# Optimization experiments

Measured on AMD Instinct MI355X. Metric: run time of the kernel, lower is better.

Reference implementation:

```python
import jax, jax.numpy as jnp
import numpy as np

P = 7            # cfg.PATCH_SIZE_PHOTOMETRIC
BRIGHT = 0.02    # bright_threshold
BIG = 1e9        # masks invalid points out of kNN
K = 5            # neighbors for smoothness/slope


def _smooth_l1(x, y, beta):
    d = jnp.abs(x - y)
    return jnp.where(d < beta, 0.5 * d * d / beta, d - 0.5 * beta)


def _sample_patches(img, kp):
    # img: [B,1,H,W], kp: [B,N,2] (x,y) in pixel coords -> [B,1,N,P,P]
    # matches F.grid_sample(align_corners=True, bilinear, border): with the
    # module's normalization, sampling positions are exactly pixel coords.
    B, _, H, W = img.shape
    N = kp.shape[1]
    half = P // 2
    lin = jnp.linspace(-half, half, P)
    oy, ox = jnp.meshgrid(lin, lin, indexing='ij')  # patch index (i,j): +x=lin[j], +y=lin[i]
    px = jnp.clip(kp[..., 0:1] + ox.ravel(), 0.0, W - 1)  # [B,N,P*P]
    py = jnp.clip(kp[..., 1:2] + oy.ravel(), 0.0, H - 1)
    x0 = jnp.floor(px); y0 = jnp.floor(py)
    fx = px - x0; fy = py - y0
    x0i = jnp.clip(x0.astype(jnp.int32), 0, W - 1)
    x1i = jnp.clip(x0i + 1, 0, W - 1)
    y0i = jnp.clip(y0.astype(jnp.int32), 0, H - 1)
    y1i = jnp.clip(y0i + 1, 0, H - 1)
    im = img[:, 0]  # [B,H,W]
    b = jnp.arange(B)[:, None, None]
    v00 = im[b, y0i, x0i]; v01 = im[b, y0i, x1i]
    v10 = im[b, y1i, x0i]; v11 = im[b, y1i, x1i]
    val = (v00 * (1 - fx) + v01 * fx) * (1 - fy) + (v10 * (1 - fx) + v11 * fx) * fy
    return val.reshape(B, 1, N, P, P)


def _forward(lg, rg, kpl, kpr, scores, Q):
    B, N, _ = kpl.shape
    # ---- epipolar ----
    y_diff = jnp.abs(kpl[..., 1] - kpr[..., 1])
    ws = scores.sum()
    l_epipolar = jnp.where(ws > 1e-4, (y_diff * scores).sum() / jnp.maximum(ws, 1e-12), y_diff.mean())
    # ---- photometric + intensity ----
    pl = _sample_patches(lg, kpl)
    pr = _sample_patches(rg, kpr)
    c = P // 2
    center_l = pl[:, 0, :, c, c]  # [B,N]
    center_r = pr[:, 0, :, c, c]
    is_bright = (center_l > BRIGHT).astype(pl.dtype)
    diff = jnp.abs(pl - pr).mean(axis=(1, 3, 4))  # [B,N]
    w = scores * is_bright
    wsum = w.sum()
    safe = jnp.maximum(wsum, 1e-12)
    l_masked = jnp.where(wsum > 1e-4, (diff * w).sum() / safe, 0.0)
    l_intensity = jnp.where(wsum > 1e-4, (_smooth_l1(center_l, center_r, 1.0) * w).sum() / safe, 0.0)
    l_photo = l_masked + l_intensity
    # ---- disparity -> 3D ----
    disp = kpl[..., 0] - kpr[..., 0]
    pts4 = jnp.concatenate([kpl, disp[..., None], jnp.ones((B, N, 1), kpl.dtype)], axis=-1)
    proj = jnp.einsum('bni,bji->bnj', pts4, Q)
    Wc = jnp.maximum(proj[..., 3], 1e-6)
    p3d = proj[..., :3] / Wc[..., None]  # [B,N,3]
    Z = p3d[..., 2]
    valid = (Z > 100) & (Z < 30000) & (scores > 0.1)  # [B,N]
    # ---- kNN smoothness / slope / zero-mean (masked, vectorized) ----
    pm = p3d / 1000.0
    xy = pm[..., jnp.array([0, 2])]  # [B,N,2] horizontal plane
    h = pm[..., 1]                   # [B,N] height
    sq = (xy * xy).sum(-1)
    d2 = sq[:, :, None] + sq[:, None, :] - 2.0 * jnp.einsum('bnd,bmd->bnm', xy, xy)
    dist = jnp.sqrt(jnp.maximum(d2, 1e-12))  # [B,N,N]
    vm = valid[:, :, None] & valid[:, None, :]
    dist = jnp.where(vm, dist, BIG)
    negd, idx = jax.lax.top_k(-dist, K + 1)   # ascending distance
    nbr_idx = idx[:, :, 1:]                   # drop self
    nbr_d = jnp.maximum(-negd[:, :, 1:], 1e-3)
    b = jnp.arange(B)[:, None, None]
    nbr_h = h[b, nbr_idx]                     # [B,N,K]
    local_mean = nbr_h.mean(-1)
    n_valid = valid.sum(-1)
    nv = jnp.maximum(n_valid, 1).astype(h.dtype)
    vf = valid.astype(h.dtype)
    ls_b = (_smooth_l1(h, local_mean, 0.01) * vf).sum(-1) / nv
    slopes = jnp.abs(nbr_h - h[..., None]) / nbr_d
    pen = jax.nn.relu(slopes - 0.4)
    lsl_b = (pen * vf[..., None]).sum((-1, -2)) / (nv * K)
    lz_b = jnp.abs((h * vf).sum(-1) / nv)
    ok = (n_valid >= 10).astype(h.dtype)
    nb = jnp.maximum(ok.sum(), 1.0)
    gate = ((scores > 0.1).sum() >= 10) & (ok.sum() > 0)
    l_smooth = jnp.where(gate, (ls_b * ok).sum() / nb, 0.0)
    l_slope = jnp.where(gate, (lsl_b * ok).sum() / nb, 0.0)
    l_zeromean = jnp.where(gate, (lz_b * ok).sum() / nb, 0.0)
    return (l_photo, l_epipolar, l_smooth, l_slope, l_zeromean)


def setup_inputs() -> dict:
    key = jax.random.key(0)
    k = jax.random.split(key, 7)
    B, N, H, W = 16, 2000, 720, 1280
    lg = jax.random.uniform(k[0], (B, 1, H, W), dtype=jnp.float32)
    rg = jax.random.uniform(k[1], (B, 1, H, W), dtype=jnp.float32)
    kx = jax.random.uniform(k[2], (B, N), minval=200.0, maxval=1080.0)
    ky = jax.random.uniform(k[3], (B, N), minval=50.0, maxval=670.0)
    disp = jax.random.uniform(k[4], (B, N), minval=10.0, maxval=200.0)
    kpl = jnp.stack([kx, ky], -1)
    kpr = jnp.stack([kx - disp, ky + 0.5 * jax.random.normal(k[5], (B, N))], -1)
    scores = jax.random.uniform(k[6], (B, N), dtype=jnp.float32)
    f, cx, cy, Tx = 1000.0, 640.0, 360.0, 120.0  # focal px, principal point, baseline mm
    Qm = jnp.array([[1.0, 0.0, 0.0, -cx],
                    [0.0, 1.0, 0.0, -cy],
                    [0.0, 0.0, 0.0, f],
                    [0.0, 0.0, 1.0 / Tx, 0.0]], dtype=jnp.float32)
    Q = jnp.broadcast_to(Qm, (B, 4, 4))
    return {"lg": lg, "rg": rg, "kpl": kpl, "kpr": kpr, "scores": scores, "Q": Q}


def reference(lg, rg, kpl, kpr, scores, Q):
    return _forward(lg, rg, kpl, kpr, scores, Q)
```

## Files before the change

kernel.cpp:

```cpp
#include <hip/hip_runtime.h>

#define BB 16
#define NN 2000
#define HH 720
#define WW 1280
#define NPT (BB*NN)
#define PATCH_BLOCKS (NPT/32)
#define PROJ_BLOCKS (NPT/256)
#define KSTRIDE 2048

static __device__ __forceinline__ unsigned u_min(unsigned a, unsigned b){ return a < b ? a : b; }

static __device__ __forceinline__ unsigned u_med3(unsigned a, unsigned b, unsigned c) {
    unsigned d;
    asm("v_med3_u32 %0, %1, %2, %3" : "=v"(d) : "v"(a), "v"(b), "v"(c));
    return d;
}

__device__ __forceinline__ void ins5(unsigned K[5], unsigned u) {
    K[4] = u_med3(K[3], K[4], u);
    K[3] = u_med3(K[2], K[3], u);
    K[2] = u_med3(K[1], K[2], u);
    K[1] = u_med3(K[0], K[1], u);
    K[0] = u_min(K[0], u);
}

__device__ __forceinline__ float bilin(const float* __restrict__ im, float px, float py) {
    px = fminf(fmaxf(px, 0.f), (float)(WW - 1));
    py = fminf(fmaxf(py, 0.f), (float)(HH - 1));
    float x0f = floorf(px), y0f = floorf(py);
    float fx = px - x0f, fy = py - y0f;
    int x0 = min(max((int)x0f, 0), WW - 1);
    int x1 = min(x0 + 1, WW - 1);
    int y0 = min(max((int)y0f, 0), HH - 1);
    int y1 = min(y0 + 1, HH - 1);
    const float* r0 = im + (size_t)y0 * WW;
    const float* r1 = im + (size_t)y1 * WW;
    float v00 = r0[x0], v01 = r0[x1], v10 = r1[x0], v11 = r1[x1];
    return (v00 * (1.f - fx) + v01 * fx) * (1.f - fy)
         + (v10 * (1.f - fx) + v11 * fx) * fy;
}

__global__ __launch_bounds__(256) void project_kernel(
    const float* __restrict__ kpl, const float* __restrict__ kpr,
    const float* __restrict__ scores, const float* __restrict__ Q,
    float4* __restrict__ pts, float* __restrict__ partialsA,
    float* __restrict__ batch_acc, unsigned* __restrict__ dcnt)
{
    if (blockIdx.x == 0) {
        if (threadIdx.x < BB * 4) batch_acc[threadIdx.x] = 0.f;
        if (threadIdx.x == BB * 4) *dcnt = 0u;
    }
    int pt = blockIdx.x * 256 + threadIdx.x;
    int b  = pt / NN;

    float2 kl = ((const float2* __restrict__)kpl)[pt];
    float2 kr = ((const float2* __restrict__)kpr)[pt];
    float sc  = scores[pt];
    float ydiff = fabsf(kl.y - kr.y);

    const float* q = Q + b * 16;
    float dsp = kl.x - kr.x;
    float p0 = q[0]*kl.x  + q[1]*kl.y  + q[2]*dsp  + q[3];
    float p1 = q[4]*kl.x  + q[5]*kl.y  + q[6]*dsp  + q[7];
    float p2 = q[8]*kl.x  + q[9]*kl.y  + q[10]*dsp + q[11];
    float p3 = q[12]*kl.x + q[13]*kl.y + q[14]*dsp + q[15];
    float Wc = fmaxf(p3, 1e-6f);
    float X = p0 / Wc, Y = p1 / Wc, Z = p2 / Wc;
    bool valid = (Z > 100.f) && (Z < 30000.f) && (sc > 0.1f);
    float x  = X / 1000.f;
    float hh = Y / 1000.f;
    float y  = Z / 1000.f;
    float sq = x * x + y * y;
    if (!valid) { x = 0.f; y = 0.f; sq = 1e18f; }
    pts[pt] = make_float4(x, y, sq, hh);

    float s0 = sc, s1 = ydiff * sc, s2 = ydiff, s3 = (sc > 0.1f) ? 1.f : 0.f;
    #pragma unroll
    for (int off = 32; off > 0; off >>= 1) {
        s0 += __shfl_down(s0, off, 64);
        s1 += __shfl_down(s1, off, 64);
        s2 += __shfl_down(s2, off, 64);
        s3 += __shfl_down(s3, off, 64);
    }
    __shared__ float red[4][4];
    int wave = threadIdx.x >> 6, lane = threadIdx.x & 63;
    if (lane == 0) { red[wave][0]=s0; red[wave][1]=s1; red[wave][2]=s2; red[wave][3]=s3; }
    __syncthreads();
    if (threadIdx.x < 4) {
        int k = threadIdx.x;
        partialsA[blockIdx.x * 4 + k] = red[0][k] + red[1][k] + red[2][k] + red[3][k];
    }
}

__global__ __launch_bounds__(256) void fused_patch_scan(
    const float* __restrict__ lg, const float* __restrict__ rg,
    const float* __restrict__ kpl, const float* __restrict__ kpr,
    const float* __restrict__ scores,
    const float4* __restrict__ pts, unsigned* __restrict__ keybuf,
    float* __restrict__ partialsB, int msegLen, int lns)
{
    if (blockIdx.x < PATCH_BLOCKS) {
        int wave = threadIdx.x >> 6, lane = threadIdx.x & 63;
        int rr = lane / 7, ci = lane - rr * 7;
        int s00 = lane + rr;
        if (s00 > 54) s00 = 54;
        int reg_r = lane >> 3, reg_c = lane & 7;

        float a3 = 0.f, a4 = 0.f, a5 = 0.f;

        for (int it = 0; it < 8; ++it) {
            int pt = blockIdx.x * 32 + wave * 8 + it;
            int b = pt / NN;
            const float* iml = lg + (size_t)b * (HH * WW);
            const float* imr = rg + (size_t)b * (HH * WW);
            float kxl = kpl[2*pt], kyl = kpl[2*pt+1];
            float kxr = kpr[2*pt], kyr = kpr[2*pt+1];
            float sc  = scores[pt];

            float flx = floorf(kxl), fly = floorf(kyl);
            int xbl = (int)flx - 3, ybl = (int)fly - 3;
            float fxl = kxl - flx, fyl = kyl - fly;
            float vl = 0.f;
            if (xbl >= 0 && xbl <= WW-8 && ybl >= 0 && ybl <= HH-8) {
                float reg = iml[(size_t)(ybl + reg_r) * WW + xbl + reg_c];
                float v00 = __shfl(reg, s00,     64);
                float v01 = __shfl(reg, s00 + 1, 64);
                float v10 = __shfl(reg, s00 + 8, 64);
                float v11 = __shfl(reg, s00 + 9, 64);
                vl = (v00*(1.f-fxl) + v01*fxl)*(1.f-fyl) + (v10*(1.f-fxl) + v11*fxl)*fyl;
            } else if (lane < 49) {
                vl = bilin(iml, kxl + (float)(ci-3), kyl + (float)(rr-3));
            }
            float frx = floorf(kxr), fry = floorf(kyr);
            int xbr = (int)frx - 3, ybr = (int)fry - 3;
            float fxr = kxr - frx, fyr = kyr - fry;
            float vr = 0.f;
            if (xbr >= 0 && xbr <= WW-8 && ybr >= 0 && ybr <= HH-8) {
                float reg = imr[(size_t)(ybr + reg_r) * WW + xbr + reg_c];
                float v00 = __shfl(reg, s00,     64);
                float v01 = __shfl(reg, s00 + 1, 64);
                float v10 = __shfl(reg, s00 + 8, 64);
                float v11 = __shfl(reg, s00 + 9, 64);
                vr = (v00*(1.f-fxr) + v01*fxr)*(1.f-fyr) + (v10*(1.f-fxr) + v11*fxr)*fyr;
            } else if (lane < 49) {
                vr = bilin(imr, kxr + (float)(ci-3), kyr + (float)(rr-3));
            }

            float adiff = (lane < 49) ? fabsf(vl - vr) : 0.f;
            float cl = __shfl(vl, 24, 64);
            float cr = __shfl(vr, 24, 64);
            #pragma unroll
            for (int off = 32; off > 0; off >>= 1) adiff += __shfl_down(adiff, off, 64);

            if (lane == 0) {
                float diff = adiff / 49.f;
                float isb  = (cl > 0.02f) ? 1.f : 0.f;
                float w    = sc * isb;
                float dc = fabsf(cl - cr);
                float sl1 = (dc < 1.f) ? 0.5f * dc * dc : dc - 0.5f;
                a3 += w;  a4 += diff * w;  a5 += sl1 * w;
            }
        }

        __shared__ float red[4][3];
        if (lane == 0) { red[wave][0]=a3; red[wave][1]=a4; red[wave][2]=a5; }
        __syncthreads();
        if (threadIdx.x < 4) {
            int k = threadIdx.x;
            float v = 0.f;
            if (k < 3) v = red[0][k] + red[1][k] + red[2][k] + red[3][k];
            partialsB[blockIdx.x * 4 + k] = v;
        }
    } else {
        int sblk = blockIdx.x - PATCH_BLOCKS;
        int bx   = sblk & 7;
        int r    = sblk >> 3;
        int seg  = r & ((1 << lns) - 1);
        int b    = r >> lns;
        int ns   = 1 << lns;
        int mseg0 = seg * msegLen;
        int n = bx * 256 + threadIdx.x;
        int nc = (n < NN) ? n : (NN - 1);

        float4 me = pts[b * NN + nc];
        float nx2 = -2.f * me.x, ny2 = -2.f * me.y, sqn = me.z;

        unsigned K[5] = {0xFFFFFFFFu,0xFFFFFFFFu,0xFFFFFFFFu,0xFFFFFFFFu,0xFFFFFFFFu};

        const float4* cand = pts + b * NN + mseg0;
        int nb0 = bx * 256;
        bool has_self = (mseg0 < nb0 + 256) && (mseg0 + msegLen > nb0);

        if (has_self) {
            #pragma unroll 5
            for (int mm = 0; mm < msegLen; ++mm) {
                float4 o = cand[mm];
                int m = mseg0 + mm;
                float t = fmaf(ny2, o.y, o.z);
                t = fmaf(nx2, o.x, t);
                float d2 = fmaxf(t + sqn, 1e-12f);
                unsigned u = (__float_as_uint(d2) & 0xFFFFF800u) | (unsigned)m;
                u = (m == n) ? 0xFFFFFFFFu : u;
                ins5(K, u);
            }
        } else {
            #pragma unroll 5
            for (int mm = 0; mm < msegLen; ++mm) {
                float4 o = cand[mm];
                int m = mseg0 + mm;
                float t = fmaf(ny2, o.y, o.z);
                t = fmaf(nx2, o.x, t);
                float d2 = fmaxf(t + sqn, 1e-12f);
                unsigned u = (__float_as_uint(d2) & 0xFFFFF800u) | (unsigned)m;
                ins5(K, u);
            }
        }

        if (n < NN) {
            size_t base = (size_t)((b * ns + seg) * 5) * KSTRIDE + n;
            keybuf[base              ] = K[0];
            keybuf[base + KSTRIDE    ] = K[1];
            keybuf[base + KSTRIDE * 2] = K[2];
            keybuf[base + KSTRIDE * 3] = K[3];
            keybuf[base + KSTRIDE * 4] = K[4];
        }
    }
}

__global__ __launch_bounds__(256) void knn_merge_final(
    const float4* __restrict__ pts, const unsigned* __restrict__ keybuf,
    float* __restrict__ batch_acc, unsigned* __restrict__ dcnt,
    const float* __restrict__ partialsA, const float* __restrict__ partialsB,
    float* __restrict__ out, int ns)
{
    int b = blockIdx.y;
    int n = blockIdx.x * 256 + threadIdx.x;

    float ls = 0.f, pen = 0.f, hacc = 0.f, cnt = 0.f;
    if (n < NN) {
        float4 me = pts[b * NN + n];
        if (me.z < 1e17f) {
            unsigned K[5] = {0xFFFFFFFFu,0xFFFFFFFFu,0xFFFFFFFFu,0xFFFFFFFFu,0xFFFFFFFFu};
            for (int s = 0; s < ns; ++s) {
                #pragma unroll
                for (int j = 0; j < 5; ++j) {
                    unsigned u = keybuf[(size_t)((b * ns + s) * 5 + j) * KSTRIDE + n];
                    ins5(K, u);
                }
            }
            float hsum = 0.f;
            #pragma unroll
            for (int t = 0; t < 5; ++t) {
                int idx = (int)(K[t] & 2047u);
                float4 o = pts[b * NN + idx];
                float dot = me.x * o.x + me.y * o.y;
                float d2 = (me.z + o.z) - 2.f * dot;
                float nd = fmaxf(sqrtf(fmaxf(d2, 1e-12f)), 0.001f);
                hsum += o.w;
                pen  += fmaxf(fabsf(o.w - me.w) / nd - 0.4f, 0.f);
            }
            float lm = hsum / 5.f;
            float dd = fabsf(me.w - lm);
            ls = (dd < 0.01f) ? 0.5f * dd * dd / 0.01f : dd - 0.005f;
            hacc = me.w;
            cnt  = 1.f;
        }
    }

    #pragma unroll
    for (int off = 32; off > 0; off >>= 1) {
        ls   += __shfl_down(ls,   off, 64);
        pen  += __shfl_down(pen,  off, 64);
        hacc += __shfl_down(hacc, off, 64);
        cnt  += __shfl_down(cnt,  off, 64);
    }
    __shared__ float r2[4][4];
    int wave = threadIdx.x >> 6, lane = threadIdx.x & 63;
    if (lane == 0) { r2[wave][0]=cnt; r2[wave][1]=ls; r2[wave][2]=pen; r2[wave][3]=hacc; }
    __syncthreads();
    if (threadIdx.x == 0) {
        float tc = r2[0][0]+r2[1][0]+r2[2][0]+r2[3][0];
        float tl = r2[0][1]+r2[1][1]+r2[2][1]+r2[3][1];
        float tp = r2[0][2]+r2[1][2]+r2[2][2]+r2[3][2];
        float th = r2[0][3]+r2[1][3]+r2[2][3]+r2[3][3];
        atomicAdd(&batch_acc[b * 4 + 0], tc);
        atomicAdd(&batch_acc[b * 4 + 1], tl);
        atomicAdd(&batch_acc[b * 4 + 2], tp);
        atomicAdd(&batch_acc[b * 4 + 3], th);
    }

    __shared__ int lastf;
    __threadfence();
    if (threadIdx.x == 0) {
        unsigned old = atomicAdd(dcnt, 1u);
        lastf = (old == (unsigned)(8 * BB - 1)) ? 1 : 0;
    }
    __syncthreads();
    if (!lastf) return;
    __threadfence();

    float s[7] = {0,0,0,0,0,0,0};
    for (int rI = threadIdx.x; rI < PROJ_BLOCKS; rI += 256) {
        s[0] += partialsA[rI * 4 + 0];
        s[1] += partialsA[rI * 4 + 1];
        s[2] += partialsA[rI * 4 + 2];
        s[3] += partialsA[rI * 4 + 3];
    }
    for (int rI = threadIdx.x; rI < PATCH_BLOCKS; rI += 256) {
        s[4] += partialsB[rI * 4 + 0];
        s[5] += partialsB[rI * 4 + 1];
        s[6] += partialsB[rI * 4 + 2];
    }
    #pragma unroll
    for (int off = 32; off > 0; off >>= 1) {
        #pragma unroll
        for (int k = 0; k < 7; ++k) s[k] += __shfl_down(s[k], off, 64);
    }
    __shared__ float ws2[4][7];
    if (lane == 0) {
        #pragma unroll
        for (int k = 0; k < 7; ++k) ws2[wave][k] = s[k];
    }
    __syncthreads();
    if (threadIdx.x == 0) {
        float t[7];
        #pragma unroll
        for (int k = 0; k < 7; ++k)
            t[k] = ws2[0][k] + ws2[1][k] + ws2[2][k] + ws2[3][k];
        float ssc = t[0], yds = t[1], yd = t[2], cnts = t[3];
        float wsum = t[4], dw = t[5], iw = t[6];

        float l_epi = (ssc > 1e-4f) ? yds / fmaxf(ssc, 1e-12f) : yd / (float)NPT;
        float safe = fmaxf(wsum, 1e-12f);
        float l_photo = (wsum > 1e-4f) ? (dw / safe + iw / safe) : 0.f;

        float als = 0.f, alsl = 0.f, alz = 0.f, okc = 0.f;
        for (int bb = 0; bb < BB; ++bb) {
            float nvf  = __hip_atomic_load(&batch_acc[bb*4+0], __ATOMIC_RELAXED, __HIP_MEMORY_SCOPE_AGENT);
            float lsb  = __hip_atomic_load(&batch_acc[bb*4+1], __ATOMIC_RELAXED, __HIP_MEMORY_SCOPE_AGENT);
            float penb = __hip_atomic_load(&batch_acc[bb*4+2], __ATOMIC_RELAXED, __HIP_MEMORY_SCOPE_AGENT);
            float hb   = __hip_atomic_load(&batch_acc[bb*4+3], __ATOMIC_RELAXED, __HIP_MEMORY_SCOPE_AGENT);
            float nv = fmaxf(nvf, 1.f);
            float ok = (nvf >= 10.f) ? 1.f : 0.f;
            als  += ok * (lsb / nv);
            alsl += ok * (penb / (nv * 5.f));
            alz  += ok * fabsf(hb / nv);
            okc  += ok;
        }
        float nb = fmaxf(okc, 1.f);
        bool gate = (cnts >= 10.f) && (okc > 0.f);
        out[0] = l_photo;
        out[1] = l_epi;
        out[2] = gate ? als / nb : 0.f;
        out[3] = gate ? alsl / nb : 0.f;
        out[4] = gate ? alz / nb : 0.f;
    }
}

extern "C" void kernel_launch(void* const* d_in, const int* in_sizes, int n_in,
                              void* d_out, int out_size, void* d_ws, size_t ws_size,
                              hipStream_t stream)
{
    const float* lg     = (const float*)d_in[0];
    const float* rg     = (const float*)d_in[1];
    const float* kpl    = (const float*)d_in[2];
    const float* kpr    = (const float*)d_in[3];
    const float* scores = (const float*)d_in[4];
    const float* Q      = (const float*)d_in[5];
    float* out = (float*)d_out;

    char* ws = (char*)d_ws;
    float4*   pts       = (float4*)ws;
    float*    partialsA = (float*)(ws + 512000);
    float*    partialsB = (float*)(ws + 514048);
    float*    batch_acc = (float*)(ws + 530432);
    unsigned* dcnt      = (unsigned*)(ws + 530688);
    unsigned* keybuf    = (unsigned*)(ws + 530944);

    int ns = 16;
    if (ws_size < 530944 + (size_t)BB * 16 * 5 * KSTRIDE * 4) ns = 8;
    if (ws_size < 530944 + (size_t)BB *  8 * 5 * KSTRIDE * 4) ns = 4;
    int lns = (ns == 16) ? 4 : ((ns == 8) ? 3 : 2);
    int msegLen = NN / ns;

    project_kernel<<<PROJ_BLOCKS, 256, 0, stream>>>(kpl, kpr, scores, Q,
                                                    pts, partialsA, batch_acc, dcnt);
    fused_patch_scan<<<PATCH_BLOCKS + 8 * ns * BB, 256, 0, stream>>>(
        lg, rg, kpl, kpr, scores, pts, keybuf, partialsB, msegLen, lns);
    knn_merge_final<<<dim3(8, BB), 256, 0, stream>>>(pts, keybuf, batch_acc, dcnt,
                                                     partialsA, partialsB, out, ns);
}
```

Baseline: 186.1 us.

## Prefetch all patch loads up front and defer per-point reductions to one wave reduce

```diff
diff --git a/kernel.cpp b/kernel.cpp
--- a/kernel.cpp
+++ b/kernel.cpp
@@ -106,11 +106,29 @@
         int s00 = lane + rr;
         if (s00 > 54) s00 = 54;
         int reg_r = lane >> 3, reg_c = lane & 7;
-
-        float a3 = 0.f, a4 = 0.f, a5 = 0.f;
-
+        int pt0 = blockIdx.x * 32 + wave * 8;
+
+        float gl[8], gr[8];
+        #pragma unroll
         for (int it = 0; it < 8; ++it) {
-            int pt = blockIdx.x * 32 + wave * 8 + it;
+            int pt = pt0 + it;
+            int b = pt / NN;
+            const float* iml = lg + (size_t)b * (HH * WW);
+            const float* imr = rg + (size_t)b * (HH * WW);
+            float kxl = kpl[2*pt], kyl = kpl[2*pt+1];
+            float kxr = kpr[2*pt], kyr = kpr[2*pt+1];
+            int xbl = (int)floorf(kxl) - 3, ybl = (int)floorf(kyl) - 3;
+            int xbr = (int)floorf(kxr) - 3, ybr = (int)floorf(kyr) - 3;
+            int xl = min(max(xbl, 0), WW - 8), yl = min(max(ybl, 0), HH - 8);
+            int xr = min(max(xbr, 0), WW - 8), yr = min(max(ybr, 0), HH - 8);
+            gl[it] = iml[(size_t)(yl + reg_r) * WW + xl + reg_c];
+            gr[it] = imr[(size_t)(yr + reg_r) * WW + xr + reg_c];
+        }
+
+        float a3 = 0.f, a4l = 0.f, a5 = 0.f;
+        #pragma unroll
+        for (int it = 0; it < 8; ++it) {
+            int pt = pt0 + it;
             int b = pt / NN;
             const float* iml = lg + (size_t)b * (HH * WW);
             const float* imr = rg + (size_t)b * (HH * WW);
@@ -121,50 +139,51 @@
             float flx = floorf(kxl), fly = floorf(kyl);
             int xbl = (int)flx - 3, ybl = (int)fly - 3;
             float fxl = kxl - flx, fyl = kyl - fly;
-            float vl = 0.f;
+            float vl;
             if (xbl >= 0 && xbl <= WW-8 && ybl >= 0 && ybl <= HH-8) {
-                float reg = iml[(size_t)(ybl + reg_r) * WW + xbl + reg_c];
-                float v00 = __shfl(reg, s00,     64);
-                float v01 = __shfl(reg, s00 + 1, 64);
-                float v10 = __shfl(reg, s00 + 8, 64);
-                float v11 = __shfl(reg, s00 + 9, 64);
+                float v00 = __shfl(gl[it], s00,     64);
+                float v01 = __shfl(gl[it], s00 + 1, 64);
+                float v10 = __shfl(gl[it], s00 + 8, 64);
+                float v11 = __shfl(gl[it], s00 + 9, 64);
                 vl = (v00*(1.f-fxl) + v01*fxl)*(1.f-fyl) + (v10*(1.f-fxl) + v11*fxl)*fyl;
-            } else if (lane < 49) {
-                vl = bilin(iml, kxl + (float)(ci-3), kyl + (float)(rr-3));
+            } else {
+                vl = 0.f;
+                if (lane < 49) vl = bilin(iml, kxl + (float)(ci-3), kyl + (float)(rr-3));
             }
             float frx = floorf(kxr), fry = floorf(kyr);
             int xbr = (int)frx - 3, ybr = (int)fry - 3;
             float fxr = kxr - frx, fyr = kyr - fry;
-            float vr = 0.f;
+            float vr;
             if (xbr >= 0 && xbr <= WW-8 && ybr >= 0 && ybr <= HH-8) {
-                float reg = imr[(size_t)(ybr + reg_r) * WW + xbr + reg_c];
-                float v00 = __shfl(reg, s00,     64);
-                float v01 = __shfl(reg, s00 + 1, 64);
-                float v10 = __shfl(reg, s00 + 8, 64);
-                float v11 = __shfl(reg, s00 + 9, 64);
+                float v00 = __shfl(gr[it], s00,     64);
+                float v01 = __shfl(gr[it], s00 + 1, 64);
+                float v10 = __shfl(gr[it], s00 + 8, 64);
+                float v11 = __shfl(gr[it], s00 + 9, 64);
                 vr = (v00*(1.f-fxr) + v01*fxr)*(1.f-fyr) + (v10*(1.f-fxr) + v11*fxr)*fyr;
-            } else if (lane < 49) {
-                vr = bilin(imr, kxr + (float)(ci-3), kyr + (float)(rr-3));
-            }
-
-            float adiff = (lane < 49) ? fabsf(vl - vr) : 0.f;
+            } else {
+                vr = 0.f;
+                if (lane < 49) vr = bilin(imr, kxr + (float)(ci-3), kyr + (float)(rr-3));
+            }
+
             float cl = __shfl(vl, 24, 64);
             float cr = __shfl(vr, 24, 64);
-            #pragma unroll
-            for (int off = 32; off > 0; off >>= 1) adiff += __shfl_down(adiff, off, 64);
-
-            if (lane == 0) {
-                float diff = adiff / 49.f;
-                float isb  = (cl > 0.02f) ? 1.f : 0.f;
-                float w    = sc * isb;
-                float dc = fabsf(cl - cr);
-                float sl1 = (dc < 1.f) ? 0.5f * dc * dc : dc - 0.5f;
-                a3 += w;  a4 += diff * w;  a5 += sl1 * w;
-            }
-        }
+            float adiff = (lane < 49) ? fabsf(vl - vr) : 0.f;
+
+            float isb = (cl > 0.02f) ? 1.f : 0.f;
+            float w   = sc * isb;
+            float dc  = fabsf(cl - cr);
+            float sl1 = (dc < 1.f) ? 0.5f * dc * dc : dc - 0.5f;
+
+            a3 += w;
+            a5 += sl1 * w;
+            a4l += w * adiff;
+        }
+
+        #pragma unroll
+        for (int off = 32; off > 0; off >>= 1) a4l += __shfl_down(a4l, off, 64);
 
         __shared__ float red[4][3];
-        if (lane == 0) { red[wave][0]=a3; red[wave][1]=a4; red[wave][2]=a5; }
+        if (lane == 0) { red[wave][0]=a3; red[wave][1]=a4l * (1.f/49.f); red[wave][2]=a5; }
         __syncthreads();
         if (threadIdx.x < 4) {
             int k = threadIdx.x;
```

After: 194.9 us. 4.7% more time.
